# Kernel optimization log

Measured on AMD Instinct MI355X. Metric: run time of the kernel, lower is better.

Reference implementation:

```python
import jax, jax.numpy as jnp
from jax import lax
import numpy as np

VQ_DIM = 64
VQ_NUM = 512


def conv1d(x, w, b=None, stride=1, pad=0):
    # x: (N, C, L), w: (O, I, K) torch Conv1d layout
    y = lax.conv_general_dilated(x, w, (stride,), [(pad, pad)],
                                 dimension_numbers=('NCH', 'OIH', 'NCH'))
    return y if b is None else y + b[None, :, None]


def convT1d(x, w, b=None, stride=1, pad=0):
    # w: (I, O, K) torch ConvTranspose1d layout; emulate via input-dilated conv
    k = w.shape[2]
    w2 = jnp.flip(w, 2).transpose(1, 0, 2)  # -> (O, I, K)
    y = lax.conv_general_dilated(x, w2, (1,), [(k - 1 - pad, k - 1 - pad)],
                                 lhs_dilation=(stride,),
                                 dimension_numbers=('NCH', 'OIH', 'NCH'))
    return y if b is None else y + b[None, :, None]


def bn(x, g, b, eps=1e-5):
    # training-mode BatchNorm1d: batch stats over (N, L), biased variance
    mu = x.mean((0, 2), keepdims=True)
    var = x.var((0, 2), keepdims=True)
    return g[None, :, None] * (x - mu) * lax.rsqrt(var + eps) + b[None, :, None]


def setup_inputs() -> dict:
    key = jax.random.key(0)
    ks = iter(jax.random.split(key, 64))

    def rn(shape, s=0.05):
        return jax.random.normal(next(ks), shape, jnp.float32) * s

    inp = {}
    inp['x'] = jax.random.normal(next(ks), (64, 32, 1024), jnp.float32)
    inp['w_conv'] = rn((64, 32, 7)); inp['b_conv'] = rn((64,))
    inp['g_conv'] = jnp.ones((64,), jnp.float32); inp['be_conv'] = jnp.zeros((64,), jnp.float32)
    inp['w_r1'] = rn((3, 64, 64, 3)); inp['b_r1'] = rn((3, 64))
    inp['g_r1'] = jnp.ones((3, 64), jnp.float32); inp['be_r1'] = jnp.zeros((3, 64), jnp.float32)
    inp['w_ds1'] = rn((64, 64, 2)); inp['b_ds1'] = rn((64,))
    inp['w_r2'] = rn((128, 64, 3)); inp['b_r2'] = rn((128,))
    inp['g_r2'] = jnp.ones((128,), jnp.float32); inp['be_r2'] = jnp.zeros((128,), jnp.float32)
    inp['w_1to2'] = rn((128, 64, 1))
    inp['w_ds2'] = rn((128, 128, 2)); inp['b_ds2'] = rn((128,))
    initrange = 1.0 / VQ_NUM
    inp['embed_w'] = jax.random.uniform(next(ks), (VQ_NUM, VQ_DIM), jnp.float32,
                                        minval=-initrange, maxval=initrange)
    inp['w_us2'] = rn((128, 128, 2)); inp['b_us2'] = rn((128,))
    inp['w_dr2'] = rn((128, 64, 3)); inp['b_dr2'] = rn((64,))
    inp['g_dr2'] = jnp.ones((64,), jnp.float32); inp['be_dr2'] = jnp.zeros((64,), jnp.float32)
    inp['w_2to1'] = rn((64, 128, 1))
    inp['w_us1'] = rn((64, 64, 2)); inp['b_us1'] = rn((64,))
    inp['w_dr1'] = rn((3, 64, 64, 3)); inp['b_dr1'] = rn((3, 64))
    inp['g_dr1'] = jnp.ones((3, 64), jnp.float32); inp['be_dr1'] = jnp.zeros((3, 64), jnp.float32)
    inp['w_deconv'] = rn((64, 32, 7)); inp['b_deconv'] = rn((32,))
    return inp


def reference(x, w_conv, b_conv, g_conv, be_conv, w_r1, b_r1, g_r1, be_r1,
              w_ds1, b_ds1, w_r2, b_r2, g_r2, be_r2, w_1to2, w_ds2, b_ds2,
              embed_w, w_us2, b_us2, w_dr2, b_dr2, g_dr2, be_dr2, w_2to1,
              w_us1, b_us1, w_dr1, b_dr1, g_dr1, be_dr1, w_deconv, b_deconv):
    # ---- encoder ----
    h = bn(conv1d(x, w_conv, b_conv, pad=3), g_conv, be_conv)
    r = h
    for i in range(3):
        r = bn(conv1d(r, w_r1[i], b_r1[i], pad=1), g_r1[i], be_r1[i])
        if i < 2:
            r = jax.nn.relu(r)
    h = h + r                                  # res1 skip
    h = conv1d(h, w_ds1, b_ds1, stride=2)      # L -> L/2
    r = bn(conv1d(h, w_r2, b_r2, pad=1), g_r2, be_r2)
    h = conv1d(h, w_1to2) + r                  # res2 skip w/ 1x1 channel map
    h = conv1d(h, w_ds2, b_ds2, stride=2)      # L/2 -> L/4
    # ---- vector quantization ----
    B, C, L = h.shape
    Z = h.reshape(-1, VQ_DIM)                  # (N, vq_dim)
    # ||z - w||^2 expanded: avoids (N, K, D) broadcast intermediate
    d = (Z * Z).sum(1, keepdims=True) - 2.0 * (Z @ embed_w.T) + (embed_w * embed_w).sum(1)[None, :]
    j = jnp.argmin(d, axis=1)
    Wj = embed_w[j]
    sg = lax.stop_gradient
    commit_loss = ((Z - sg(Wj)) ** 2).sum(1).mean()
    vq_loss = ((sg(Z) - Wj) ** 2).sum(1).mean()
    hq = Wj.reshape(B, C, L)
    # ---- decoder ----
    t = convT1d(hq, w_us2, b_us2, stride=2)    # L/4 -> L/2
    r = bn(convT1d(t, w_dr2, b_dr2, pad=1), g_dr2, be_dr2)
    t = conv1d(t, w_2to1) + r
    t = convT1d(t, w_us1, b_us1, stride=2)     # L/2 -> L
    r = t
    for i in range(3):
        r = bn(convT1d(r, w_dr1[i], b_dr1[i], pad=1), g_dr1[i], be_dr1[i])
        if i < 2:
            r = jax.nn.relu(r)
    t = t + r
    out = convT1d(t, w_deconv, b_deconv, pad=3)
    return out, commit_loss, vq_loss
```

## Files before the change

### kernel.cpp

```cpp
#include <hip/hip_runtime.h>
#include <stdint.h>

#define F_WT     1
#define F_STATS  2
#define F_BIAS   4
#define F_INBN   8
#define F_INRELU 16
#define F_INB    32
#define F_INBBN  64
#define F_ADD    128
#define F_ADDBN  256

template<int CI, int CO, int K, int MODE, int TL, int COB, int CR, int PAD,
         int FLAGS>
__global__ __launch_bounds__(256)
void conv_rI(const float* __restrict__ xa, const float2* __restrict__ sca,
             const float* __restrict__ xb, const float2* __restrict__ scb,
             const float* __restrict__ w,  const float* __restrict__ bias,
             const float* __restrict__ addsrc, const float2* __restrict__ scadd,
             double* __restrict__ stats, float* __restrict__ yout,
             int Lin, int Lout, int cis, int wci)
{
    constexpr int NCG  = COB / CR;
    constexpr int LT   = 256 / NCG;
    constexpr int TLT  = TL / LT;
    constexpr int SPAN = (MODE == 0) ? (TL + K - 1)
                       : (MODE == 1) ? ((TL - 1) * 2 + K)
                       : (TL / 2);
    constexpr int SPANP = (SPAN + 3) & ~3;
    constexpr int WR    = K * CR;
    constexpr int WRP   = (WR + 3) & ~3;
    constexpr int WROW  = CI * WRP + 4;
    constexpr int XR    = (MODE == 0) ? (TLT + K - 1)
                        : (MODE == 1) ? ((TLT - 1) * 2 + K)
                        : (TLT / 2);
    constexpr int ALN  = (MODE == 0) ? ((4 - (PAD & 3)) & 3) : 0;
    constexpr int NW   = (SPAN + ALN + 3) / 4;
    constexpr int NTASK = CI * NW;
    constexpr int PT    = (NTASK + 255) / 256;
    constexpr bool F4ST = (ALN == 0) && (SPAN % 4 == 0);
    constexpr int WNT   = NCG * CI * WR;
    constexpr int WPT   = (WNT + 255) / 256;

    __shared__ float xs[CI * SPANP];
    __shared__ float wl[NCG * WROW];

    const int tid    = threadIdx.x;
    const int ltile  = blockIdx.x;
    const int n      = blockIdx.y;
    const int coBase = blockIdx.z * COB;

    {
        float wvv[WPT];
#pragma unroll
        for (int p = 0; p < WPT; ++p) {
            int i = tid + p * 256;
            float v = 0.f;
            if (i < WNT) {
                int cogi = i / (CI * WR);
                int rem  = i - cogi * (CI * WR);
                int ci   = rem / WR;
                int rem2 = rem - ci * WR;
                int k    = rem2 / CR;
                int cr   = rem2 - k * CR;
                int co   = coBase + cogi * CR + cr;
                int src;
                if (FLAGS & F_WT)   src = (ci * CO + co) * K + (K - 1 - k);
                else if (MODE == 2) src = (ci * CO + co) * K + k;
                else                src = (co * wci + ci) * K + k;
                v = w[src];
            }
            wvv[p] = v;
        }
#pragma unroll
        for (int p = 0; p < WPT; ++p) {
            int i = tid + p * 256;
            if (i < WNT) {
                int cogi = i / (CI * WR);
                int rem  = i - cogi * (CI * WR);
                int ci   = rem / WR;
                int rem2 = rem - ci * WR;
                int k    = rem2 / CR;
                int cr   = rem2 - k * CR;
                wl[cogi * WROW + ci * WRP + k * CR + cr] = wvv[p];
            }
        }
    }

    int x0;
    if (MODE == 0)      x0 = ltile * TL - PAD;
    else if (MODE == 1) x0 = ltile * TL * 2;
    else                x0 = ltile * (TL / 2);
    const int xw0 = x0 - ALN;

    {
        float4 va[PT];
        float4 vb[PT];
#pragma unroll
        for (int p = 0; p < PT; ++p) {
            int i = tid + p * 256;
            float4 v = make_float4(0.f, 0.f, 0.f, 0.f);
            float4 u = make_float4(0.f, 0.f, 0.f, 0.f);
            if (i < NTASK) {
                int ci  = i / NW;
                int q   = i - ci * NW;
                int xl4 = xw0 + 4 * q;
                size_t rb = ((size_t)n * cis + ci) * (size_t)Lin;
                if (xl4 >= 0 && xl4 + 3 < Lin) {
                    v = *(const float4*)(xa + rb + xl4);
                    if (FLAGS & F_INB) u = *(const float4*)(xb + rb + xl4);
                } else {
                    float* pv = (float*)&v;
                    float* pu = (float*)&u;
#pragma unroll
                    for (int t = 0; t < 4; ++t) {
                        int xl = xl4 + t;
                        if (xl >= 0 && xl < Lin) {
                            pv[t] = xa[rb + xl];
                            if (FLAGS & F_INB) pu[t] = xb[rb + xl];
                        }
                    }
                }
            }
            va[p] = v;
            if (FLAGS & F_INB) vb[p] = u;
        }
#pragma unroll
        for (int p = 0; p < PT; ++p) {
            int i = tid + p * 256;
            if (i < NTASK) {
                int ci = i / NW;
                int q  = i - ci * NW;
                int xl4 = xw0 + 4 * q;
                float4 v = va[p];
                float* pv = (float*)&v;
                if (FLAGS & F_INBN) {
                    float2 t = sca[ci];
#pragma unroll
                    for (int e = 0; e < 4; ++e) pv[e] = pv[e] * t.x + t.y;
                }
                if (FLAGS & F_INRELU) {
#pragma unroll
                    for (int e = 0; e < 4; ++e) pv[e] = fmaxf(pv[e], 0.f);
                }
                if (FLAGS & F_INB) {
                    float4 u = vb[p];
                    float* pu = (float*)&u;
                    if (FLAGS & F_INBBN) {
                        float2 t = scb[ci];
#pragma unroll
                        for (int e = 0; e < 4; ++e) {
                            float uu = pu[e] * t.x + t.y;
                            pv[e] += uu;
                        }
                    } else {
#pragma unroll
                        for (int e = 0; e < 4; ++e) pv[e] += pu[e];
                    }
                }
#pragma unroll
                for (int e = 0; e < 4; ++e) {
                    int xl = xl4 + e;
                    if (xl < 0 || xl >= Lin) pv[e] = 0.f;
                }
                if constexpr (F4ST) {
                    *(float4*)&xs[ci * SPANP + 4 * q] = v;
                } else {
#pragma unroll
                    for (int t = 0; t < 4; ++t) {
                        int s = 4 * q + t - ALN;
                        if (s >= 0 && s < SPAN) xs[ci * SPANP + s] = pv[t];
                    }
                }
            }
        }
    }
    __syncthreads();

    const int cog   = tid / LT;
    const int lg    = tid % LT;
    const int co0   = coBase + cog * CR;
    const int loOff = lg * TLT;
    const int xoff  = (MODE == 1) ? loOff * 2
                    : (MODE == 2) ? (loOff >> 1) : loOff;

    float acc[CR][TLT];
#pragma unroll
    for (int cr = 0; cr < CR; ++cr) {
        float b = (FLAGS & F_BIAS) ? bias[co0 + cr] : 0.f;
#pragma unroll
        for (int j = 0; j < TLT; ++j) acc[cr][j] = b;
    }

    float xA[XR], xB[XR], wA[WR], wB[WR];

    auto ldx = [&](float* dst, int c) {
        const int base = c * SPANP + xoff;
#pragma unroll
        for (int g = 0; g < XR; g += 4) {
            const float* p = &xs[base + g];
#pragma unroll
            for (int t = 0; t < 4; ++t)
                if (g + t < XR) dst[g + t] = p[t];
        }
    };
    auto ldw = [&](float* dst, int c) {
        const float* q = &wl[cog * WROW + c * WRP];
#pragma unroll
        for (int t = 0; t < WR; ++t) dst[t] = q[t];
    };
    auto dofma = [&](const float* xv, const float* wv) {
        if (MODE == 2) {
#pragma unroll
            for (int j = 0; j < TLT; ++j)
#pragma unroll
                for (int cr = 0; cr < CR; ++cr)
                    acc[cr][j] += wv[(j & 1) * CR + cr] * xv[j >> 1];
        } else {
#pragma unroll
            for (int k = 0; k < K; ++k)
#pragma unroll
                for (int j = 0; j < TLT; ++j)
#pragma unroll
                    for (int cr = 0; cr < CR; ++cr)
                        acc[cr][j] += wv[k * CR + cr]
                                    * xv[((MODE == 1) ? 2 * j : j) + k];
        }
    };

    if constexpr (K <= 3) {
        ldx(xA, 0); ldw(wA, 0);
        for (int ci = 0; ci + 2 < CI; ci += 2) {
            ldx(xB, ci + 1); ldw(wB, ci + 1);
            dofma(xA, wA);
            ldx(xA, ci + 2); ldw(wA, ci + 2);
            dofma(xB, wB);
        }
        ldx(xB, CI - 1); ldw(wB, CI - 1);
        dofma(xA, wA);
        dofma(xB, wB);
    } else {
#pragma unroll 2
        for (int ci = 0; ci < CI; ++ci) {
            ldx(xA, ci); ldw(wA, ci);
            dofma(xA, wA);
        }
    }

    const int lo0 = ltile * TL + loOff;
#pragma unroll
    for (int cr = 0; cr < CR; ++cr) {
        size_t ob = ((size_t)n * CO + (co0 + cr)) * (size_t)Lout + lo0;
        if (FLAGS & F_ADD) {
            float2 t = (FLAGS & F_ADDBN) ? scadd[co0 + cr] : make_float2(1.f, 0.f);
            if constexpr (TLT % 4 == 0) {
#pragma unroll
                for (int jv = 0; jv < TLT / 4; ++jv) {
                    float4 av = ((const float4*)(addsrc + ob))[jv];
                    float* a4 = &acc[cr][jv * 4];
                    if (FLAGS & F_ADDBN) {
                        a4[0] += av.x * t.x + t.y; a4[1] += av.y * t.x + t.y;
                        a4[2] += av.z * t.x + t.y; a4[3] += av.w * t.x + t.y;
                    } else {
                        a4[0] += av.x; a4[1] += av.y; a4[2] += av.z; a4[3] += av.w;
                    }
                }
            } else {
#pragma unroll
                for (int j = 0; j < TLT; ++j) {
                    float a = addsrc[ob + j];
                    acc[cr][j] += (FLAGS & F_ADDBN) ? (a * t.x + t.y) : a;
                }
            }
        }
        if constexpr (TLT % 4 == 0) {
#pragma unroll
            for (int jv = 0; jv < TLT / 4; ++jv) {
                float4 sv = make_float4(acc[cr][jv*4+0], acc[cr][jv*4+1],
                                        acc[cr][jv*4+2], acc[cr][jv*4+3]);
                ((float4*)(yout + ob))[jv] = sv;
            }
        } else {
#pragma unroll
            for (int j = 0; j < TLT; ++j) yout[ob + j] = acc[cr][j];
        }
    }

    if (FLAGS & F_STATS) {
        float s1[CR], s2[CR];
#pragma unroll
        for (int cr = 0; cr < CR; ++cr) {
            s1[cr] = 0.f; s2[cr] = 0.f;
#pragma unroll
            for (int j = 0; j < TLT; ++j) {
                s1[cr] += acc[cr][j];
                s2[cr] += acc[cr][j] * acc[cr][j];
            }
        }
#pragma unroll
        for (int m = 1; m < LT; m <<= 1) {
#pragma unroll
            for (int cr = 0; cr < CR; ++cr) {
                s1[cr] += __shfl_xor(s1[cr], m, 64);
                s2[cr] += __shfl_xor(s2[cr], m, 64);
            }
        }
        if ((tid & (LT - 1)) == 0) {
#pragma unroll
            for (int cr = 0; cr < CR; ++cr) {
                atomicAdd(&stats[co0 + cr],      (double)s1[cr]);
                atomicAdd(&stats[CO + co0 + cr], (double)s2[cr]);
            }
        }
    }
}

__global__ void bnp_rD(const double* __restrict__ stats,
                       const float* __restrict__ g, const float* __restrict__ be,
                       float2* __restrict__ sc, int C, double invNL)
{
    int c = threadIdx.x;
    if (c >= C) return;
    double mu  = stats[c] * invNL;
    double var = stats[C + c] * invNL - mu * mu;
    double rs  = 1.0 / sqrt(var + 1e-5);
    double gv  = (double)g[c] * rs;
    double bv  = (double)be[c] - mu * gv;
    sc[c] = make_float2((float)gv, (float)bv);
}

__global__ __launch_bounds__(256)
void vq1_rF(const float* __restrict__ z, const float* __restrict__ emb,
            float* __restrict__ d0, float* __restrict__ d1,
            int* __restrict__ j0, int* __restrict__ j1)
{
    __shared__ float ws[128 * 68];
    const int tid  = threadIdx.x;
    const int sub  = tid & 3;
    const int half = blockIdx.x & 1;
    const int r    = (blockIdx.x >> 1) * 64 + (tid >> 2);

    const float4* zp = (const float4*)(z + (size_t)r * 64 + sub * 16);
    float4 z0 = zp[0], z1 = zp[1], z2 = zp[2], z3 = zp[3];

    float zzp = 0.f;
    zzp = fmaf(z0.x,z0.x,zzp); zzp = fmaf(z0.y,z0.y,zzp);
    zzp = fmaf(z0.z,z0.z,zzp); zzp = fmaf(z0.w,z0.w,zzp);
    zzp = fmaf(z1.x,z1.x,zzp); zzp = fmaf(z1.y,z1.y,zzp);
    zzp = fmaf(z1.z,z1.z,zzp); zzp = fmaf(z1.w,z1.w,zzp);
    zzp = fmaf(z2.x,z2.x,zzp); zzp = fmaf(z2.y,z2.y,zzp);
    zzp = fmaf(z2.z,z2.z,zzp); zzp = fmaf(z2.w,z2.w,zzp);
    zzp = fmaf(z3.x,z3.x,zzp); zzp = fmaf(z3.y,z3.y,zzp);
    zzp = fmaf(z3.z,z3.z,zzp); zzp = fmaf(z3.w,z3.w,zzp);

    float best = 3.4e38f;
    int   bj   = 0;
    for (int cc = 0; cc < 2; ++cc) {
        const int c0 = half * 256 + cc * 128;
        __syncthreads();
        for (int i = tid; i < 128 * 16; i += 256) {
            int j = i >> 4, q = i & 15;
            ((float4*)ws)[j * 17 + q] = ((const float4*)(emb + c0 * 64))[i];
        }
        __syncthreads();
        for (int i = tid; i < 512; i += 256) {
            int j = i >> 2, s = i & 3;
            const float4* p = (const float4*)&ws[j * 68 + s * 16];
            float4 a = p[0], b = p[1], c = p[2], d = p[3];
            float ww = 0.f;
            ww = fmaf(a.x,a.x,ww); ww = fmaf(a.y,a.y,ww);
            ww = fmaf(a.z,a.z,ww); ww = fmaf(a.w,a.w,ww);
            ww = fmaf(b.x,b.x,ww); ww = fmaf(b.y,b.y,ww);
            ww = fmaf(b.z,b.z,ww); ww = fmaf(b.w,b.w,ww);
            ww = fmaf(c.x,c.x,ww); ww = fmaf(c.y,c.y,ww);
            ww = fmaf(c.z,c.z,ww); ww = fmaf(c.w,c.w,ww);
            ww = fmaf(d.x,d.x,ww); ww = fmaf(d.y,d.y,ww);
            ww = fmaf(d.z,d.z,ww); ww = fmaf(d.w,d.w,ww);
            ws[j * 68 + 64 + s] = ww;
        }
        __syncthreads();
        for (int j = 0; j < 128; ++j) {
            const float4* wp = (const float4*)&ws[j * 68 + sub * 16];
            float4 w0 = wp[0], w1 = wp[1], w2 = wp[2], w3 = wp[3];
            float dot = 0.f;
            dot = fmaf(z0.x,w0.x,dot); dot = fmaf(z0.y,w0.y,dot);
            dot = fmaf(z0.z,w0.z,dot); dot = fmaf(z0.w,w0.w,dot);
            dot = fmaf(z1.x,w1.x,dot); dot = fmaf(z1.y,w1.y,dot);
            dot = fmaf(z1.z,w1.z,dot); dot = fmaf(z1.w,w1.w,dot);
            dot = fmaf(z2.x,w2.x,dot); dot = fmaf(z2.y,w2.y,dot);
            dot = fmaf(z2.z,w2.z,dot); dot = fmaf(z2.w,w2.w,dot);
            dot = fmaf(z3.x,w3.x,dot); dot = fmaf(z3.y,w3.y,dot);
            dot = fmaf(z3.z,w3.z,dot); dot = fmaf(z3.w,w3.w,dot);
            float t = fmaf(dot, -2.f, ws[j * 68 + 64 + sub]);
            t += __shfl_xor(t, 1, 64);
            t += __shfl_xor(t, 2, 64);
            if (t < best) { best = t; bj = c0 + j; }
        }
    }

    float zz = zzp;
    zz += __shfl_xor(zz, 1, 64);
    zz += __shfl_xor(zz, 2, 64);

    if (sub == 0) {
        if (half) { d1[r] = zz + best; j1[r] = bj; }
        else      { d0[r] = zz + best; j0[r] = bj; }
    }
}

__global__ __launch_bounds__(256)
void vq2_rF(const float* __restrict__ d0, const float* __restrict__ d1,
            const int* __restrict__ j0, const int* __restrict__ j1,
            const float* __restrict__ emb, float* __restrict__ hq,
            double* __restrict__ lossAcc)
{
    const int r = blockIdx.x * 256 + threadIdx.x;
    float da = d0[r], db = d1[r];
    bool pick1 = db < da;
    float d = pick1 ? db : da;
    int   j = pick1 ? j1[r] : j0[r];

    const float4* ep = (const float4*)(emb + (size_t)j * 64);
    float4* hp = (float4*)(hq + (size_t)r * 64);
#pragma unroll
    for (int t = 0; t < 16; ++t) hp[t] = ep[t];

    float s = d;
#pragma unroll
    for (int m = 1; m < 64; m <<= 1) s += __shfl_xor(s, m, 64);
    if ((threadIdx.x & 63) == 0) atomicAdd(lossAcc, (double)s);
}

__global__ void zd_rD(double* p, int n) {
    int i = blockIdx.x * 256 + threadIdx.x;
    if (i < n) p[i] = 0.0;
}

__global__ void wsguard_rD(float* p, int n) {
    int i = blockIdx.x * 256 + threadIdx.x;
    if (i < n) p[i] = 1000.0f;
}

__global__ void lossfin_rD(const double* acc, float* out) {
    float m = (float)(acc[0] * (1.0 / 32768.0));
    out[2097152] = m;
    out[2097153] = m;
}

extern "C" void kernel_launch(void* const* d_in, const int* in_sizes, int n_in,
                              void* d_out, int out_size, void* d_ws, size_t ws_size,
                              hipStream_t stream)
{
    const size_t NEED = (size_t)3 * 4194304 * 4 + 2305 * 8 + 1152 * 8 + 64;
    if (ws_size < NEED) {
        wsguard_rD<<<dim3((out_size + 255) / 256), 256, 0, stream>>>((float*)d_out, out_size);
        return;
    }

    const float* x        = (const float*)d_in[0];
    const float* w_conv   = (const float*)d_in[1];
    const float* b_conv   = (const float*)d_in[2];
    const float* g_conv   = (const float*)d_in[3];
    const float* be_conv  = (const float*)d_in[4];
    const float* w_r1     = (const float*)d_in[5];
    const float* b_r1     = (const float*)d_in[6];
    const float* g_r1     = (const float*)d_in[7];
    const float* be_r1    = (const float*)d_in[8];
    const float* w_ds1    = (const float*)d_in[9];
    const float* b_ds1    = (const float*)d_in[10];
    const float* w_r2     = (const float*)d_in[11];
    const float* b_r2     = (const float*)d_in[12];
    const float* g_r2     = (const float*)d_in[13];
    const float* be_r2    = (const float*)d_in[14];
    const float* w_1to2   = (const float*)d_in[15];
    const float* w_ds2    = (const float*)d_in[16];
    const float* b_ds2    = (const float*)d_in[17];
    const float* embed_w  = (const float*)d_in[18];
    const float* w_us2    = (const float*)d_in[19];
    const float* b_us2    = (const float*)d_in[20];
    const float* w_dr2    = (const float*)d_in[21];
    const float* b_dr2    = (const float*)d_in[22];
    const float* g_dr2    = (const float*)d_in[23];
    const float* be_dr2   = (const float*)d_in[24];
    const float* w_2to1   = (const float*)d_in[25];
    const float* w_us1    = (const float*)d_in[26];
    const float* b_us1    = (const float*)d_in[27];
    const float* w_dr1    = (const float*)d_in[28];
    const float* b_dr1    = (const float*)d_in[29];
    const float* g_dr1    = (const float*)d_in[30];
    const float* be_dr1   = (const float*)d_in[31];
    const float* w_deconv = (const float*)d_in[32];
    const float* b_deconv = (const float*)d_in[33];

    float* out = (float*)d_out;

    float*  B0 = (float*)d_ws;
    float*  B1 = B0 + 4194304;
    float*  B2 = B1 + 4194304;
    double* SD = (double*)(B2 + 4194304);
    double* lossAcc = SD + 9 * 256;
    float2* SC = (float2*)(SD + 2305);

    float* vqd0 = B0;
    float* vqd1 = B0 + 32768;
    int*   vqj0 = (int*)(B0 + 65536);
    int*   vqj1 = (int*)(B0 + 98304);

    const int N = 64;
    const double i64k = 1.0 / 65536.0;
    const double i32k = 1.0 / 32768.0;
    const float2* NOSC = nullptr;
    const float*  NOP  = nullptr;

    zd_rD<<<dim3(10), 256, 0, stream>>>(SD, 9 * 256 + 1);

    conv_rI<32,64,7,0,128,32,4,3, F_BIAS|F_STATS>
        <<<dim3(8, N, 2), 256, 0, stream>>>(x, NOSC, NOP, NOSC, w_conv, b_conv,
            NOP, NOSC, SD+0*256, B0, 1024, 1024, 32, 32);
    bnp_rD<<<1, 128, 0, stream>>>(SD+0*256, g_conv, be_conv, SC+0*128, 64, i64k);

    conv_rI<64,64,3,0,128,32,4,1, F_BIAS|F_STATS|F_INBN>
        <<<dim3(8, N, 2), 256, 0, stream>>>(B0, SC+0*128, NOP, NOSC, w_r1, b_r1,
            NOP, NOSC, SD+1*256, B1, 1024, 1024, 64, 64);
    bnp_rD<<<1, 128, 0, stream>>>(SD+1*256, g_r1, be_r1, SC+1*128, 64, i64k);

    conv_rI<64,64,3,0,128,32,4,1, F_BIAS|F_STATS|F_INBN|F_INRELU>
        <<<dim3(8, N, 2), 256, 0, stream>>>(B1, SC+1*128, NOP, NOSC, w_r1+12288, b_r1+64,
            NOP, NOSC, SD+2*256, B2, 1024, 1024, 64, 64);
    bnp_rD<<<1, 128, 0, stream>>>(SD+2*256, g_r1+64, be_r1+64, SC+2*128, 64, i64k);

    conv_rI<64,64,3,0,128,32,4,1, F_BIAS|F_STATS|F_INBN|F_INRELU>
        <<<dim3(8, N, 2), 256, 0, stream>>>(B2, SC+2*128, NOP, NOSC, w_r1+24576, b_r1+128,
            NOP, NOSC, SD+3*256, B1, 1024, 1024, 64, 64);
    bnp_rD<<<1, 128, 0, stream>>>(SD+3*256, g_r1+128, be_r1+128, SC+3*128, 64, i64k);

    conv_rI<64,64,2,1,64,32,4,0, F_BIAS|F_INBN|F_INB|F_INBBN>
        <<<dim3(8, N, 2), 256, 0, stream>>>(B1, SC+3*128, B0, SC+0*128, w_ds1, b_ds1,
            NOP, NOSC, nullptr, B2, 1024, 512, 64, 64);

    conv_rI<64,128,3,0,128,32,4,1, F_BIAS|F_STATS>
        <<<dim3(4, N, 4), 256, 0, stream>>>(B2, NOSC, NOP, NOSC, w_r2, b_r2,
            NOP, NOSC, SD+4*256, B1, 512, 512, 64, 64);
    bnp_rD<<<1, 128, 0, stream>>>(SD+4*256, g_r2, be_r2, SC+4*128, 128, i32k);

    conv_rI<64,128,1,0,128,32,4,0, F_ADD|F_ADDBN>
        <<<dim3(4, N, 4), 256, 0, stream>>>(B2, NOSC, NOP, NOSC, w_1to2, NOP,
            B1, SC+4*128, nullptr, B0, 512, 512, 64, 64);

    conv_rI<128,128,2,1,32,32,4,0, F_BIAS>
        <<<dim3(8, N, 4), 256, 0, stream>>>(B0, NOSC, NOP, NOSC, w_ds2, b_ds2,
            NOP, NOSC, nullptr, B1, 512, 256, 128, 128);

    vq1_rF<<<dim3(1024), 256, 0, stream>>>(B1, embed_w, vqd0, vqd1, vqj0, vqj1);
    vq2_rF<<<dim3(128), 256, 0, stream>>>(vqd0, vqd1, vqj0, vqj1, embed_w, B2, lossAcc);
    lossfin_rD<<<1, 1, 0, stream>>>(lossAcc, out);

    conv_rI<128,128,2,2,128,32,4,0, F_BIAS>
        <<<dim3(4, N, 4), 256, 0, stream>>>(B2, NOSC, NOP, NOSC, w_us2, b_us2,
            NOP, NOSC, nullptr, B0, 256, 512, 128, 128);

    conv_rI<64,64,3,0,128,32,4,1, F_WT|F_BIAS>
        <<<dim3(4, N, 2), 256, 0, stream>>>(B0, NOSC, NOP, NOSC, w_dr2, b_dr2,
            NOP, NOSC, nullptr, B1, 512, 512, 128, 64);
    conv_rI<64,64,3,0,128,32,4,1, F_WT|F_STATS|F_ADD>
        <<<dim3(4, N, 2), 256, 0, stream>>>(B0 + (size_t)64*512, NOSC, NOP, NOSC,
            w_dr2 + 64*64*3, NOP, B1, NOSC, SD+5*256, B1, 512, 512, 128, 64);
    bnp_rD<<<1, 128, 0, stream>>>(SD+5*256, g_dr2, be_dr2, SC+5*128, 64, i32k);

    conv_rI<64,64,1,0,128,32,4,0, F_ADD|F_ADDBN>
        <<<dim3(4, N, 2), 256, 0, stream>>>(B0, NOSC, NOP, NOSC, w_2to1, NOP,
            B1, SC+5*128, nullptr, B2, 512, 512, 128, 128);
    conv_rI<64,64,1,0,128,32,4,0, F_ADD>
        <<<dim3(4, N, 2), 256, 0, stream>>>(B0 + (size_t)64*512, NOSC, NOP, NOSC,
            w_2to1 + 64, NOP, B2, NOSC, nullptr, B2, 512, 512, 128, 128);

    conv_rI<64,64,2,2,128,32,4,0, F_BIAS>
        <<<dim3(8, N, 2), 256, 0, stream>>>(B2, NOSC, NOP, NOSC, w_us1, b_us1,
            NOP, NOSC, nullptr, B0, 512, 1024, 64, 64);

    conv_rI<64,64,3,0,128,32,4,1, F_WT|F_BIAS|F_STATS>
        <<<dim3(8, N, 2), 256, 0, stream>>>(B0, NOSC, NOP, NOSC, w_dr1, b_dr1,
            NOP, NOSC, SD+6*256, B1, 1024, 1024, 64, 64);
    bnp_rD<<<1, 128, 0, stream>>>(SD+6*256, g_dr1, be_dr1, SC+6*128, 64, i64k);

    conv_rI<64,64,3,0,128,32,4,1, F_WT|F_BIAS|F_STATS|F_INBN|F_INRELU>
        <<<dim3(8, N, 2), 256, 0, stream>>>(B1, SC+6*128, NOP, NOSC, w_dr1+12288, b_dr1+64,
            NOP, NOSC, SD+7*256, B2, 1024, 1024, 64, 64);
    bnp_rD<<<1, 128, 0, stream>>>(SD+7*256, g_dr1+64, be_dr1+64, SC+7*128, 64, i64k);

    conv_rI<64,64,3,0,128,32,4,1, F_WT|F_BIAS|F_STATS|F_INBN|F_INRELU>
        <<<dim3(8, N, 2), 256, 0, stream>>>(B2, SC+7*128, NOP, NOSC, w_dr1+24576, b_dr1+128,
            NOP, NOSC, SD+8*256, B1, 1024, 1024, 64, 64);
    bnp_rD<<<1, 128, 0, stream>>>(SD+8*256, g_dr1+128, be_dr1+128, SC+8*128, 64, i64k);

    conv_rI<64,32,7,0,128,16,4,3, F_WT|F_BIAS|F_INBN|F_INB>
        <<<dim3(8, N, 2), 256, 0, stream>>>(B1, SC+8*128, B0, NOSC, w_deconv, b_deconv,
            NOP, NOSC, nullptr, out, 1024, 1024, 64, 64);
}
```

Before: 1.215 ms.

## Slab conv weight staging in LDS and deepen register pipeline over input channels

The conv kernel now stages weights into shared memory in input-channel slabs (SLABS=1 or 2), which shrinks the weight LDS footprint so more blocks can fit per CU. A launch-bounds minimum of 3 blocks per CU is requested. The inner loop now uses a 4-deep (or 2-deep for K=7) rotating register pipeline of x/w loads instead of the old double buffer. The costs are extra __syncthreads and weight reloads between slabs, and the deeper pipeline plus the occupancy bound may force register spills.

```diff
diff --git a/kernel.cpp b/kernel.cpp
--- a/kernel.cpp
+++ b/kernel.cpp
@@ -12,9 +12,9 @@
 #define F_ADDBN  256
 
 template<int CI, int CO, int K, int MODE, int TL, int COB, int CR, int PAD,
-         int FLAGS>
-__global__ __launch_bounds__(256)
-void conv_rI(const float* __restrict__ xa, const float2* __restrict__ sca,
+         int SLABS, int FLAGS>
+__global__ __launch_bounds__(256, 3)
+void conv_rJ(const float* __restrict__ xa, const float2* __restrict__ sca,
              const float* __restrict__ xb, const float2* __restrict__ scb,
              const float* __restrict__ w,  const float* __restrict__ bias,
              const float* __restrict__ addsrc, const float2* __restrict__ scadd,
@@ -27,20 +27,20 @@
     constexpr int SPAN = (MODE == 0) ? (TL + K - 1)
                        : (MODE == 1) ? ((TL - 1) * 2 + K)
                        : (TL / 2);
-    constexpr int SPANP = (SPAN + 3) & ~3;
-    constexpr int WR    = K * CR;
-    constexpr int WRP   = (WR + 3) & ~3;
-    constexpr int WROW  = CI * WRP + 4;
-    constexpr int XR    = (MODE == 0) ? (TLT + K - 1)
-                        : (MODE == 1) ? ((TLT - 1) * 2 + K)
-                        : (TLT / 2);
+    constexpr int SPANP  = (SPAN + 3) & ~3;
+    constexpr int WR     = K * CR;
+    constexpr int WRP    = (WR + 3) & ~3;
+    constexpr int SLABCI = CI / SLABS;
+    constexpr int WROW   = SLABCI * WRP + 4;
+    constexpr int XR     = (MODE == 0) ? (TLT + K - 1)
+                         : (MODE == 1) ? ((TLT - 1) * 2 + K)
+                         : (TLT / 2);
+    constexpr int PIPE   = (K >= 7) ? 2 : 4;
     constexpr int ALN  = (MODE == 0) ? ((4 - (PAD & 3)) & 3) : 0;
     constexpr int NW   = (SPAN + ALN + 3) / 4;
     constexpr int NTASK = CI * NW;
     constexpr int PT    = (NTASK + 255) / 256;
     constexpr bool F4ST = (ALN == 0) && (SPAN % 4 == 0);
-    constexpr int WNT   = NCG * CI * WR;
-    constexpr int WPT   = (WNT + 255) / 256;
 
     __shared__ float xs[CI * SPANP];
     __shared__ float wl[NCG * WROW];
@@ -50,20 +50,23 @@
     const int n      = blockIdx.y;
     const int coBase = blockIdx.z * COB;
 
-    {
+    auto stage_w = [&](int slab) {
+        constexpr int WNT = NCG * SLABCI * WR;
+        constexpr int WPT = (WNT + 255) / 256;
         float wvv[WPT];
 #pragma unroll
         for (int p = 0; p < WPT; ++p) {
             int i = tid + p * 256;
             float v = 0.f;
             if (i < WNT) {
-                int cogi = i / (CI * WR);
-                int rem  = i - cogi * (CI * WR);
-                int ci   = rem / WR;
-                int rem2 = rem - ci * WR;
+                int cogi = i / (SLABCI * WR);
+                int rem  = i - cogi * (SLABCI * WR);
+                int cil  = rem / WR;
+                int rem2 = rem - cil * WR;
                 int k    = rem2 / CR;
                 int cr   = rem2 - k * CR;
                 int co   = coBase + cogi * CR + cr;
+                int ci   = slab * SLABCI + cil;
                 int src;
                 if (FLAGS & F_WT)   src = (ci * CO + co) * K + (K - 1 - k);
                 else if (MODE == 2) src = (ci * CO + co) * K + k;
@@ -76,16 +79,14 @@
         for (int p = 0; p < WPT; ++p) {
             int i = tid + p * 256;
             if (i < WNT) {
-                int cogi = i / (CI * WR);
-                int rem  = i - cogi * (CI * WR);
-                int ci   = rem / WR;
-                int rem2 = rem - ci * WR;
-                int k    = rem2 / CR;
-                int cr   = rem2 - k * CR;
-                wl[cogi * WROW + ci * WRP + k * CR + cr] = wvv[p];
-            }
-        }
-    }
+                int cogi = i / (SLABCI * WR);
+                int rem  = i - cogi * (SLABCI * WR);
+                int cil  = rem / WR;
+                int rem2 = rem - cil * WR;
+                wl[cogi * WROW + cil * WRP + rem2] = wvv[p];
+            }
+        }
+    };
 
     int x0;
     if (MODE == 0)      x0 = ltile * TL - PAD;
@@ -125,6 +126,7 @@
             va[p] = v;
             if (FLAGS & F_INB) vb[p] = u;
         }
+        stage_w(0);
 #pragma unroll
         for (int p = 0; p < PT; ++p) {
             int i = tid + p * 256;
@@ -192,8 +194,6 @@
         for (int j = 0; j < TLT; ++j) acc[cr][j] = b;
     }
 
-    float xA[XR], xB[XR], wA[WR], wB[WR];
-
     auto ldx = [&](float* dst, int c) {
         const int base = c * SPANP + xoff;
 #pragma unroll
@@ -204,8 +204,8 @@
                 if (g + t < XR) dst[g + t] = p[t];
         }
     };
-    auto ldw = [&](float* dst, int c) {
-        const float* q = &wl[cog * WROW + c * WRP];
+    auto ldw = [&](float* dst, int cil) {
+        const float* q = &wl[cog * WROW + cil * WRP];
 #pragma unroll
         for (int t = 0; t < WR; ++t) dst[t] = q[t];
     };
@@ -228,23 +228,29 @@
         }
     };
 
-    if constexpr (K <= 3) {
-        ldx(xA, 0); ldw(wA, 0);
-        for (int ci = 0; ci + 2 < CI; ci += 2) {
-            ldx(xB, ci + 1); ldw(wB, ci + 1);
-            dofma(xA, wA);
-            ldx(xA, ci + 2); ldw(wA, ci + 2);
-            dofma(xB, wB);
-        }
-        ldx(xB, CI - 1); ldw(wB, CI - 1);
-        dofma(xA, wA);
-        dofma(xB, wB);
-    } else {
-#pragma unroll 2
-        for (int ci = 0; ci < CI; ++ci) {
-            ldx(xA, ci); ldw(wA, ci);
-            dofma(xA, wA);
-        }
+    float xP[PIPE][XR], wP[PIPE][WR];
+#pragma unroll
+    for (int s = 0; s < SLABS; ++s) {
+        if (s > 0) {
+            __syncthreads();
+            stage_w(s);
+            __syncthreads();
+        }
+#pragma unroll
+        for (int p = 0; p < PIPE; ++p) {
+            ldx(xP[p], s * SLABCI + p);
+            ldw(wP[p], p);
+        }
+        for (int cc0 = 0; cc0 < SLABCI - PIPE; cc0 += PIPE) {
+#pragma unroll
+            for (int j = 0; j < PIPE; ++j) {
+                dofma(xP[j], wP[j]);
+                ldx(xP[j], s * SLABCI + cc0 + PIPE + j);
+                ldw(wP[j], cc0 + PIPE + j);
+            }
+        }
+#pragma unroll
+        for (int j = 0; j < PIPE; ++j) dofma(xP[j], wP[j]);
     }
 
     const int lo0 = ltile * TL + loOff;
@@ -514,40 +520,40 @@
 
     zd_rD<<<dim3(10), 256, 0, stream>>>(SD, 9 * 256 + 1);
 
-    conv_rI<32,64,7,0,128,32,4,3, F_BIAS|F_STATS>
+    conv_rJ<32,64,7,0,128,32,4,3,1, F_BIAS|F_STATS>
         <<<dim3(8, N, 2), 256, 0, stream>>>(x, NOSC, NOP, NOSC, w_conv, b_conv,
             NOP, NOSC, SD+0*256, B0, 1024, 1024, 32, 32);
     bnp_rD<<<1, 128, 0, stream>>>(SD+0*256, g_conv, be_conv, SC+0*128, 64, i64k);
 
-    conv_rI<64,64,3,0,128,32,4,1, F_BIAS|F_STATS|F_INBN>
+    conv_rJ<64,64,3,0,128,32,4,1,2, F_BIAS|F_STATS|F_INBN>
         <<<dim3(8, N, 2), 256, 0, stream>>>(B0, SC+0*128, NOP, NOSC, w_r1, b_r1,
             NOP, NOSC, SD+1*256, B1, 1024, 1024, 64, 64);
     bnp_rD<<<1, 128, 0, stream>>>(SD+1*256, g_r1, be_r1, SC+1*128, 64, i64k);
 
-    conv_rI<64,64,3,0,128,32,4,1, F_BIAS|F_STATS|F_INBN|F_INRELU>
+    conv_rJ<64,64,3,0,128,32,4,1,2, F_BIAS|F_STATS|F_INBN|F_INRELU>
         <<<dim3(8, N, 2), 256, 0, stream>>>(B1, SC+1*128, NOP, NOSC, w_r1+12288, b_r1+64,
             NOP, NOSC, SD+2*256, B2, 1024, 1024, 64, 64);
     bnp_rD<<<1, 128, 0, stream>>>(SD+2*256, g_r1+64, be_r1+64, SC+2*128, 64, i64k);
 
-    conv_rI<64,64,3,0,128,32,4,1, F_BIAS|F_STATS|F_INBN|F_INRELU>
+    conv_rJ<64,64,3,0,128,32,4,1,2, F_BIAS|F_STATS|F_INBN|F_INRELU>
         <<<dim3(8, N, 2), 256, 0, stream>>>(B2, SC+2*128, NOP, NOSC, w_r1+24576, b_r1+128,
             NOP, NOSC, SD+3*256, B1, 1024, 1024, 64, 64);
     bnp_rD<<<1, 128, 0, stream>>>(SD+3*256, g_r1+128, be_r1+128, SC+3*128, 64, i64k);
 
-    conv_rI<64,64,2,1,64,32,4,0, F_BIAS|F_INBN|F_INB|F_INBBN>
+    conv_rJ<64,64,2,1,64,32,4,0,1, F_BIAS|F_INBN|F_INB|F_INBBN>
         <<<dim3(8, N, 2), 256, 0, stream>>>(B1, SC+3*128, B0, SC+0*128, w_ds1, b_ds1,
             NOP, NOSC, nullptr, B2, 1024, 512, 64, 64);
 
-    conv_rI<64,128,3,0,128,32,4,1, F_BIAS|F_STATS>
+    conv_rJ<64,128,3,0,128,32,4,1,2, F_BIAS|F_STATS>
         <<<dim3(4, N, 4), 256, 0, stream>>>(B2, NOSC, NOP, NOSC, w_r2, b_r2,
             NOP, NOSC, SD+4*256, B1, 512, 512, 64, 64);
     bnp_rD<<<1, 128, 0, stream>>>(SD+4*256, g_r2, be_r2, SC+4*128, 128, i32k);
 
-    conv_rI<64,128,1,0,128,32,4,0, F_ADD|F_ADDBN>
+    conv_rJ<64,128,1,0,128,32,4,0,1, F_ADD|F_ADDBN>
         <<<dim3(4, N, 4), 256, 0, stream>>>(B2, NOSC, NOP, NOSC, w_1to2, NOP,
             B1, SC+4*128, nullptr, B0, 512, 512, 64, 64);
 
-    conv_rI<128,128,2,1,32,32,4,0, F_BIAS>
+    conv_rJ<128,128,2,1,32,32,4,0,2, F_BIAS>
         <<<dim3(8, N, 4), 256, 0, stream>>>(B0, NOSC, NOP, NOSC, w_ds2, b_ds2,
             NOP, NOSC, nullptr, B1, 512, 256, 128, 128);
 
@@ -555,45 +561,45 @@
     vq2_rF<<<dim3(128), 256, 0, stream>>>(vqd0, vqd1, vqj0, vqj1, embed_w, B2, lossAcc);
     lossfin_rD<<<1, 1, 0, stream>>>(lossAcc, out);
 
-    conv_rI<128,128,2,2,128,32,4,0, F_BIAS>
+    conv_rJ<128,128,2,2,128,32,4,0,2, F_BIAS>
         <<<dim3(4, N, 4), 256, 0, stream>>>(B2, NOSC, NOP, NOSC, w_us2, b_us2,
             NOP, NOSC, nullptr, B0, 256, 512, 128, 128);
 
-    conv_rI<64,64,3,0,128,32,4,1, F_WT|F_BIAS>
+    conv_rJ<64,64,3,0,128,32,4,1,2, F_WT|F_BIAS>
         <<<dim3(4, N, 2), 256, 0, stream>>>(B0, NOSC, NOP, NOSC, w_dr2, b_dr2,
             NOP, NOSC, nullptr, B1, 512, 512, 128, 64);
-    conv_rI<64,64,3,0,128,32,4,1, F_WT|F_STATS|F_ADD>
+    conv_rJ<64,64,3,0,128,32,4,1,2, F_WT|F_STATS|F_ADD>
         <<<dim3(4, N, 2), 256, 0, stream>>>(B0 + (size_t)64*512, NOSC, NOP, NOSC,
             w_dr2 + 64*64*3, NOP, B1, NOSC, SD+5*256, B1, 512, 512, 128, 64);
     bnp_rD<<<1, 128, 0, stream>>>(SD+5*256, g_dr2, be_dr2, SC+5*128, 64, i32k);
 
-    conv_rI<64,64,1,0,128,32,4,0, F_ADD|F_ADDBN>
+    conv_rJ<64,64,1,0,128,32,4,0,1, F_ADD|F_ADDBN>
         <<<dim3(4, N, 2), 256, 0, stream>>>(B0, NOSC, NOP, NOSC, w_2to1, NOP,
             B1, SC+5*128, nullptr, B2, 512, 512, 128, 128);
-    conv_rI<64,64,1,0,128,32,4,0, F_ADD>
+    conv_rJ<64,64,1,0,128,32,4,0,1, F_ADD>
         <<<dim3(4, N, 2), 256, 0, stream>>>(B0 + (size_t)64*512, NOSC, NOP, NOSC,
             w_2to1 + 64, NOP, B2, NOSC, nullptr, B2, 512, 512, 128, 128);
 
-    conv_rI<64,64,2,2,128,32,4,0, F_BIAS>
+    conv_rJ<64,64,2,2,128,32,4,0,1, F_BIAS>
         <<<dim3(8, N, 2), 256, 0, stream>>>(B2, NOSC, NOP, NOSC, w_us1, b_us1,
             NOP, NOSC, nullptr, B0, 512, 1024, 64, 64);
 
-    conv_rI<64,64,3,0,128,32,4,1, F_WT|F_BIAS|F_STATS>
+    conv_rJ<64,64,3,0,128,32,4,1,2, F_WT|F_BIAS|F_STATS>
         <<<dim3(8, N, 2), 256, 0, stream>>>(B0, NOSC, NOP, NOSC, w_dr1, b_dr1,
             NOP, NOSC, SD+6*256, B1, 1024, 1024, 64, 64);
     bnp_rD<<<1, 128, 0, stream>>>(SD+6*256, g_dr1, be_dr1, SC+6*128, 64, i64k);
 
-    conv_rI<64,64,3,0,128,32,4,1, F_WT|F_BIAS|F_STATS|F_INBN|F_INRELU>
+    conv_rJ<64,64,3,0,128,32,4,1,2, F_WT|F_BIAS|F_STATS|F_INBN|F_INRELU>
         <<<dim3(8, N, 2), 256, 0, stream>>>(B1, SC+6*128, NOP, NOSC, w_dr1+12288, b_dr1+64,
             NOP, NOSC, SD+7*256, B2, 1024, 1024, 64, 64);
     bnp_rD<<<1, 128, 0, stream>>>(SD+7*256, g_dr1+64, be_dr1+64, SC+7*128, 64, i64k);
 
-    conv_rI<64,64,3,0,128,32,4,1, F_WT|F_BIAS|F_STATS|F_INBN|F_INRELU>
+    conv_rJ<64,64,3,0,128,32,4,1,2, F_WT|F_BIAS|F_STATS|F_INBN|F_INRELU>
         <<<dim3(8, N, 2), 256, 0, stream>>>(B2, SC+7*128, NOP, NOSC, w_dr1+24576, b_dr1+128,
             NOP, NOSC, SD+8*256, B1, 1024, 1024, 64, 64);
     bnp_rD<<<1, 128, 0, stream>>>(SD+8*256, g_dr1+128, be_dr1+128, SC+8*128, 64, i64k);
 
-    conv_rI<64,32,7,0,128,16,4,3, F_WT|F_BIAS|F_INBN|F_INB>
+    conv_rJ<64,32,7,0,128,16,4,3,2, F_WT|F_BIAS|F_INBN|F_INB>
         <<<dim3(8, N, 2), 256, 0, stream>>>(B1, SC+8*128, B0, NOSC, w_deconv, b_deconv,
             NOP, NOSC, nullptr, out, 1024, 1024, 64, 64);
 }
```

Result: slower. 3.857 ms (+217.3%).
